# Optimization experiments

Measured on AMD Instinct MI355X. Metric: run time of the kernel, lower is better.

The kernel has to match this reference:

```python
import jax, jax.numpy as jnp
import numpy as np

B, T, C, H = 4, 2048, 1024, 16
D = C // H  # head_size = 64


def setup_inputs() -> dict:
    key = jax.random.key(0)
    k1, k2, k3 = jax.random.split(key, 3)
    x = jax.random.normal(k1, (B, T, C), dtype=jnp.float32)
    w_qkv = jax.random.normal(k2, (C, 3 * C), dtype=jnp.float32) * (C ** -0.5)
    b_qkv = jnp.zeros((3 * C,), dtype=jnp.float32)
    w_proj = jax.random.normal(k3, (C, C), dtype=jnp.float32) * (C ** -0.5)
    b_proj = jnp.zeros((C,), dtype=jnp.float32)
    return {"x": x, "w_qkv": w_qkv, "b_qkv": b_qkv, "w_proj": w_proj, "b_proj": b_proj}


def reference(x, w_qkv, b_qkv, w_proj, b_proj):
    b, t, c = x.shape
    qkv = x @ w_qkv + b_qkv                      # [B,T,3C]
    q, k, v = jnp.split(qkv, 3, axis=-1)
    # [B,T,C] -> [B,H,T,D]
    q = q.reshape(b, t, H, D).transpose(0, 2, 1, 3)
    k = k.reshape(b, t, H, D).transpose(0, 2, 1, 3)
    v = v.reshape(b, t, H, D).transpose(0, 2, 1, 3)
    attn = jnp.einsum('bhqd,bhkd->bhqk', q, k) * (D ** -0.5)
    causal = jnp.tril(jnp.ones((t, t), dtype=bool))
    attn = jnp.where(causal[None, None], attn, -jnp.inf)
    attn = jax.nn.softmax(attn, axis=-1)
    # dropout: eval mode (identity)
    out = jnp.einsum('bhqk,bhkd->bhqd', attn, v)
    out = out.transpose(0, 2, 1, 3).reshape(b, t, c)
    return out @ w_proj + b_proj
```

## Files before the change

### kernel.cpp

```cpp
#include <hip/hip_runtime.h>

#define B_ 4
#define T_ 2048
#define C_ 1024
#define H_ 16
#define D_ 64

typedef __attribute__((ext_vector_type(8))) short short8;
typedef __attribute__((ext_vector_type(4))) float f32x4;

__device__ inline unsigned short f2bf(float f) {
    union { float f; unsigned u; } v; v.f = f;
    unsigned r = v.u + 0x7fffu + ((v.u >> 16) & 1u);
    return (unsigned short)(r >> 16);
}

__device__ inline unsigned int pk_bf16(float a, float b) {
#if __has_builtin(__builtin_amdgcn_cvt_pk_bf16_f32)
    typedef __attribute__((ext_vector_type(2))) __bf16 bf16x2;
    bf16x2 v = __builtin_amdgcn_cvt_pk_bf16_f32(a, b);
    return __builtin_bit_cast(unsigned int, v);
#else
    return (unsigned)f2bf(a) | ((unsigned)f2bf(b) << 16);
#endif
}

__device__ inline void async_ld16(const void* g, void* lds) {
    __builtin_amdgcn_global_load_lds(
        (const __attribute__((address_space(1))) unsigned int*)g,
        (__attribute__((address_space(3))) unsigned int*)lds, 16, 0, 0);
}

#define MFMA_BF16 __builtin_amdgcn_mfma_f32_16x16x32_bf16

__global__ __launch_bounds__(256) void prep_all(
    const float* __restrict__ x, const float* __restrict__ w_qkv,
    const float* __restrict__ w_proj,
    unsigned short* __restrict__ xb, unsigned short* __restrict__ wqkvT,
    unsigned short* __restrict__ wprojT)
{
    const int bid = blockIdx.x;
    if (bid < 8192) {
        int i = (bid * 256 + threadIdx.x) * 4;
        float4 v = *(const float4*)(x + i);
        uint2 o;
        o.x = pk_bf16(v.x, v.y);
        o.y = pk_bf16(v.z, v.w);
        *(uint2*)(xb + i) = o;
        return;
    }
    __shared__ float tile[32][33];
    const int tt = bid - 8192;
    int bx = tt & 127;
    const int by = tt >> 7;
    const float* src; unsigned short* dst; int Cc;
    if (bx < 96) { src = w_qkv;  dst = wqkvT;  Cc = 3072; }
    else         { src = w_proj; dst = wprojT; Cc = 1024; bx -= 96; }
    const int tx = threadIdx.x & 31, ty = threadIdx.x >> 5;
    #pragma unroll
    for (int r = 0; r < 32; r += 8)
        tile[ty + r][tx] = src[(size_t)(by*32 + ty + r) * Cc + bx*32 + tx];
    __syncthreads();
    #pragma unroll
    for (int r = 0; r < 32; r += 8)
        dst[(size_t)(bx*32 + ty + r) * 1024 + by*32 + tx] = f2bf(tile[tx][ty + r]);
}

__global__ __launch_bounds__(256) void gemm_qkv(
    const unsigned short* __restrict__ A,
    const unsigned short* __restrict__ BT,
    const float* __restrict__ bias,
    unsigned short* __restrict__ qb, unsigned short* __restrict__ kb,
    unsigned short* __restrict__ vtb)
{
    __shared__ unsigned short As[128 * 64];
    __shared__ unsigned short Bs[128 * 64];
    const int tid = threadIdx.x;
    const int wave = tid >> 6, lane = tid & 63;
    const int wm = wave >> 1, wn = wave & 1;
    const int l15 = lane & 15, lq = lane >> 4;
    const int bid = blockIdx.x;
    const int xcd = bid & 7, idx = bid >> 3;
    const int m0 = (xcd * 8 + (idx & 7)) * 128;
    const int n0 = (idx >> 3) * 128;
    const int sel = n0 >> 10;
    const int row8 = lane >> 3;
    const int chx8 = ((lane & 7) ^ row8) * 8;
    const int cxa = l15 & 7;

    f32x4 acc[4][4] = {};

    for (int k0 = 0; k0 < 1024; k0 += 64) {
        #pragma unroll
        for (int c = 0; c < 4; ++c) {
            const int r = wave*32 + c*8;
            async_ld16(A  + (size_t)(m0 + r + row8)*1024 + k0 + chx8,
                       (char*)As + r*128);
            async_ld16(BT + (size_t)(n0 + r + row8)*1024 + k0 + chx8,
                       (char*)Bs + r*128);
        }
        __syncthreads();
        #pragma unroll
        for (int ks = 0; ks < 2; ++ks) {
            short8 af[4], bf[4];
            #pragma unroll
            for (int i = 0; i < 4; ++i) {
                const int ra = wm*64 + i*16 + l15;
                const int rb = wn*64 + i*16 + l15;
                af[i] = *(const short8*)&As[ra*64 + (((ks*4 + lq) ^ cxa) << 3)];
                bf[i] = *(const short8*)&Bs[rb*64 + (((ks*4 + lq) ^ cxa) << 3)];
            }
            if (sel < 2) {
                #pragma unroll
                for (int mi = 0; mi < 4; ++mi)
                    #pragma unroll
                    for (int ni = 0; ni < 4; ++ni)
                        acc[mi][ni] = MFMA_BF16(bf[ni], af[mi], acc[mi][ni], 0, 0, 0);
            } else {
                #pragma unroll
                for (int mi = 0; mi < 4; ++mi)
                    #pragma unroll
                    for (int ni = 0; ni < 4; ++ni)
                        acc[mi][ni] = MFMA_BF16(af[mi], bf[ni], acc[mi][ni], 0, 0, 0);
            }
        }
        __syncthreads();
    }

    if (sel < 2) {
        const float qs = (sel == 0) ? 0.180336880f : 1.0f;
        unsigned short* dst = (sel == 0) ? qb : kb;
        #pragma unroll
        for (int mi = 0; mi < 4; ++mi) {
            const int t = m0 + wm*64 + mi*16 + l15;
            const int bb = t >> 11, tt = t & 2047;
            #pragma unroll
            for (int ni = 0; ni < 4; ++ni) {
                const int nb = n0 + wn*64 + ni*16 + lq*4;
                const int hh = (nb >> 6) & 15, d0 = nb & 63;
                float4 bv = *(const float4*)(bias + nb);
                float v0 = (acc[mi][ni][0] + bv.x) * qs;
                float v1 = (acc[mi][ni][1] + bv.y) * qs;
                float v2 = (acc[mi][ni][2] + bv.z) * qs;
                float v3 = (acc[mi][ni][3] + bv.w) * qs;
                uint2 pk; pk.x = pk_bf16(v0, v1); pk.y = pk_bf16(v2, v3);
                *(uint2*)(dst + ((size_t)(bb*16 + hh)*2048 + tt)*64 + d0) = pk;
            }
        }
    } else {
        #pragma unroll
        for (int mi = 0; mi < 4; ++mi) {
            const int t0 = m0 + wm*64 + mi*16 + lq*4;
            const int bb = t0 >> 11, tt = t0 & 2047;
            const int tl = tt & 63;
            const int tp = (tt & ~63) | (tl & 32) | ((tl & 12) << 1) | ((tl & 16) >> 2);
            #pragma unroll
            for (int ni = 0; ni < 4; ++ni) {
                const int n = n0 + wn*64 + ni*16 + l15;
                const int hh = (n >> 6) & 15, d = n & 63;
                const float bs = bias[n];
                uint2 pk;
                pk.x = pk_bf16(acc[mi][ni][0] + bs, acc[mi][ni][1] + bs);
                pk.y = pk_bf16(acc[mi][ni][2] + bs, acc[mi][ni][3] + bs);
                *(uint2*)(vtb + ((size_t)(bb*16 + hh)*64 + d)*2048 + tp) = pk;
            }
        }
    }
}

__global__ __launch_bounds__(256) void gemm_proj(
    const unsigned short* __restrict__ A,
    const unsigned short* __restrict__ BT,
    const float* __restrict__ bias,
    float* __restrict__ out)
{
    __shared__ unsigned short As[128 * 64];
    __shared__ unsigned short Bs[128 * 64];
    const int tid = threadIdx.x;
    const int wave = tid >> 6, lane = tid & 63;
    const int wm = wave >> 1, wn = wave & 1;
    const int l15 = lane & 15, lq = lane >> 4;
    const int bid = blockIdx.x;
    const int xcd = bid & 7, idx = bid >> 3;
    const int m0 = (xcd * 8 + (idx & 7)) * 128;
    const int n0 = (idx >> 3) * 128;
    const int row8 = lane >> 3;
    const int chx8 = ((lane & 7) ^ row8) * 8;
    const int cxa = l15 & 7;

    f32x4 acc[4][4] = {};

    for (int k0 = 0; k0 < 1024; k0 += 64) {
        #pragma unroll
        for (int c = 0; c < 4; ++c) {
            const int r = wave*32 + c*8;
            async_ld16(A  + (size_t)(m0 + r + row8)*1024 + k0 + chx8,
                       (char*)As + r*128);
            async_ld16(BT + (size_t)(n0 + r + row8)*1024 + k0 + chx8,
                       (char*)Bs + r*128);
        }
        __syncthreads();
        #pragma unroll
        for (int ks = 0; ks < 2; ++ks) {
            short8 af[4], bf[4];
            #pragma unroll
            for (int i = 0; i < 4; ++i) {
                const int ra = wm*64 + i*16 + l15;
                const int rb = wn*64 + i*16 + l15;
                af[i] = *(const short8*)&As[ra*64 + (((ks*4 + lq) ^ cxa) << 3)];
                bf[i] = *(const short8*)&Bs[rb*64 + (((ks*4 + lq) ^ cxa) << 3)];
            }
            #pragma unroll
            for (int mi = 0; mi < 4; ++mi)
                #pragma unroll
                for (int ni = 0; ni < 4; ++ni)
                    acc[mi][ni] = MFMA_BF16(bf[ni], af[mi], acc[mi][ni], 0, 0, 0);
        }
        __syncthreads();
    }

    #pragma unroll
    for (int mi = 0; mi < 4; ++mi) {
        const int m = m0 + wm*64 + mi*16 + l15;
        #pragma unroll
        for (int ni = 0; ni < 4; ++ni) {
            const int nb = n0 + wn*64 + ni*16 + lq*4;
            float4 bv = *(const float4*)(bias + nb);
            float4 o;
            o.x = acc[mi][ni][0] + bv.x;
            o.y = acc[mi][ni][1] + bv.y;
            o.z = acc[mi][ni][2] + bv.z;
            o.w = acc[mi][ni][3] + bv.w;
            *(float4*)(out + (size_t)m * 1024 + nb) = o;
        }
    }
}

__global__ __launch_bounds__(256, 2) void attn_mfma(
    const unsigned short* __restrict__ qb,
    const unsigned short* __restrict__ kb,
    const unsigned short* __restrict__ vtb,
    unsigned short* __restrict__ ab)
{
    extern __shared__ unsigned char smem[];
    const int tid  = threadIdx.x;
    const int wave = tid >> 6, lane = tid & 63;
    const int l15  = lane & 15, lq = lane >> 4;
    const int linear = blockIdx.x;
    const int xc  = linear & 7;
    const int idx = linear >> 3;
    const int bh  = xc * 8 + (idx & 7);
    const int qblk = 31 - (idx >> 3);
    const int q0 = qblk * 64;
    const int b = bh >> 4, h = bh & 15;
    const size_t base = (size_t)bh * 2048 * 64;

    unsigned short* Kw = (unsigned short*)(smem + wave * 16384);
    unsigned short* Vw = Kw + 4096;

    const int row8 = lane >> 3;
    const int chx8 = ((lane & 7) ^ row8) * 8;

#define STAGE_K(J0) do { _Pragma("unroll") for (int op = 0; op < 8; ++op) \
    async_ld16(kb + base + (size_t)((J0) + op*8 + row8)*64 + chx8, \
               (char*)Kw + op*1024); } while (0)
#define STAGE_V(J0) do { _Pragma("unroll") for (int op = 0; op < 8; ++op) \
    async_ld16(vtb + base + (size_t)(op*8 + row8)*2048 + (J0) + chx8, \
               (char*)Vw + op*1024); } while (0)

    short8 qf[2][4];
    #pragma unroll
    for (int ks = 0; ks < 2; ++ks)
        #pragma unroll
        for (int nq = 0; nq < 4; ++nq)
            qf[ks][nq] = *(const short8*)(qb + base
                + (size_t)(q0 + nq*16 + l15)*64 + ks*32 + lq*8);

    f32x4 o[4][4] = {};
    float lacc[4] = {0.f, 0.f, 0.f, 0.f};

    const int jfirst = wave * 64;
    const int nt = (qblk >= wave) ? ((qblk - wave) >> 2) + 1 : 0;

    if (nt > 0) { STAGE_K(jfirst); STAGE_V(jfirst); }

    for (int i = 0; i < nt; ++i) {
        const int j0 = jfirst + i * 256;
        const bool more = (i + 1 < nt);

        asm volatile("s_waitcnt vmcnt(8)" ::: "memory");

        short8 kf0[4], kf1[4];
        #pragma unroll
        for (int ni = 0; ni < 4; ++ni) {
            const unsigned short* kr = Kw + (ni*16 + l15) * 64;
            kf0[ni] = *(const short8*)(kr + (((0*4 + lq) ^ (l15 & 7)) << 3));
            kf1[ni] = *(const short8*)(kr + (((1*4 + lq) ^ (l15 & 7)) << 3));
        }
        f32x4 s[4][4] = {};
        #pragma unroll
        for (int ni = 0; ni < 4; ++ni)
            #pragma unroll
            for (int nq = 0; nq < 4; ++nq) {
                s[ni][nq] = MFMA_BF16(kf0[ni], qf[0][nq], s[ni][nq], 0, 0, 0);
                s[ni][nq] = MFMA_BF16(kf1[ni], qf[1][nq], s[ni][nq], 0, 0, 0);
            }
        asm volatile("s_waitcnt lgkmcnt(0)" ::: "memory");
        if (more) STAGE_K(j0 + 256);

        if (j0 == q0) {
            #pragma unroll
            for (int ni = 0; ni < 4; ++ni)
                #pragma unroll
                for (int nq = 0; nq < 4; ++nq)
                    #pragma unroll
                    for (int r = 0; r < 4; ++r)
                        if (ni*16 + lq*4 + r > nq*16 + l15)
                            s[ni][nq][r] = -1e30f;
        }

        short8 pf[2][4];
        #pragma unroll
        for (int c = 0; c < 2; ++c)
            #pragma unroll
            for (int nq = 0; nq < 4; ++nq) {
                float p0 = __builtin_amdgcn_exp2f(s[2*c  ][nq][0]);
                float p1 = __builtin_amdgcn_exp2f(s[2*c  ][nq][1]);
                float p2 = __builtin_amdgcn_exp2f(s[2*c  ][nq][2]);
                float p3 = __builtin_amdgcn_exp2f(s[2*c  ][nq][3]);
                float p4 = __builtin_amdgcn_exp2f(s[2*c+1][nq][0]);
                float p5 = __builtin_amdgcn_exp2f(s[2*c+1][nq][1]);
                float p6 = __builtin_amdgcn_exp2f(s[2*c+1][nq][2]);
                float p7 = __builtin_amdgcn_exp2f(s[2*c+1][nq][3]);
                lacc[nq] += ((p0 + p1) + (p2 + p3)) + ((p4 + p5) + (p6 + p7));
                uint4 pu;
                pu.x = pk_bf16(p0, p1); pu.y = pk_bf16(p2, p3);
                pu.z = pk_bf16(p4, p5); pu.w = pk_bf16(p6, p7);
                pf[c][nq] = __builtin_bit_cast(short8, pu);
            }

        if (more) asm volatile("s_waitcnt vmcnt(8)" ::: "memory");
        else      asm volatile("s_waitcnt vmcnt(0)" ::: "memory");

        #pragma unroll
        for (int c = 0; c < 2; ++c) {
            short8 vf[4];
            #pragma unroll
            for (int nd = 0; nd < 4; ++nd)
                vf[nd] = *(const short8*)(Vw + (nd*16 + l15) * 64
                    + (((c*4 + lq) ^ (l15 & 7)) << 3));
            #pragma unroll
            for (int nq = 0; nq < 4; ++nq)
                #pragma unroll
                for (int nd = 0; nd < 4; ++nd)
                    o[nq][nd] = MFMA_BF16(pf[c][nq], vf[nd], o[nq][nd], 0, 0, 0);
        }
        asm volatile("s_waitcnt lgkmcnt(0)" ::: "memory");
        if (more) STAGE_V(j0 + 256);
    }
#undef STAGE_K
#undef STAGE_V

    #pragma unroll
    for (int nq = 0; nq < 4; ++nq) {
        float t = lacc[nq];
        t += __shfl_xor(t, 16);
        t += __shfl_xor(t, 32);
        if (lq == 0) ((float*)Kw)[nq*16 + l15] = t;
    }
    __syncthreads();
    const int qg = wave, d = lane;
    f32x4 linv4[4];
    #pragma unroll
    for (int j = 0; j < 4; ++j) {
        f32x4 lsum = {};
        #pragma unroll
        for (int w2 = 0; w2 < 4; ++w2)
            lsum += *(const f32x4*)((const float*)(smem + w2*16384) + qg*16 + j*4);
        #pragma unroll
        for (int r = 0; r < 4; ++r)
            linv4[j][r] = __builtin_amdgcn_rcpf(lsum[r]);
    }
    __syncthreads();
    #pragma unroll
    for (int nq = 0; nq < 4; ++nq)
        #pragma unroll
        for (int nd = 0; nd < 4; ++nd) {
            const int row = nd*16 + l15;
            const int col = (nq*16 + lq*4 + 4*l15) & 63;
            *(f32x4*)((float*)Kw + row*64 + col) = o[nq][nd];
        }
    __syncthreads();
    #pragma unroll
    for (int j = 0; j < 4; ++j) {
        const int colb = (qg*16 + j*4 + 4*(d & 15)) & 63;
        f32x4 acc = {};
        #pragma unroll
        for (int w2 = 0; w2 < 4; ++w2)
            acc += *(const f32x4*)((const float*)(smem + w2*16384) + d*64 + colb);
        #pragma unroll
        for (int r = 0; r < 4; ++r) {
            const int q = qg*16 + j*4 + r;
            ab[(size_t)(b*2048 + q0 + q)*1024 + h*64 + d] = f2bf(acc[r] * linv4[j][r]);
        }
    }
}

extern "C" void kernel_launch(void* const* d_in, const int* in_sizes, int n_in,
                              void* d_out, int out_size, void* d_ws, size_t ws_size,
                              hipStream_t stream) {
    const float* x      = (const float*)d_in[0];
    const float* w_qkv  = (const float*)d_in[1];
    const float* b_qkv  = (const float*)d_in[2];
    const float* w_proj = (const float*)d_in[3];
    const float* b_proj = (const float*)d_in[4];
    float* out = (float*)d_out;

    unsigned short* xb     = (unsigned short*)d_ws;
    unsigned short* wqkvT  = xb + 8388608;
    unsigned short* wprojT = wqkvT + 3145728;
    unsigned short* qbuf   = wprojT + 1048576;
    unsigned short* kbuf   = qbuf + 8388608;
    unsigned short* vtbuf  = kbuf + 8388608;
    unsigned short* abuf   = vtbuf + 8388608;

    prep_all<<<12288, 256, 0, stream>>>(x, w_qkv, w_proj, xb, wqkvT, wprojT);
    gemm_qkv<<<1536, 256, 0, stream>>>(xb, wqkvT, b_qkv, qbuf, kbuf, vtbuf);
    attn_mfma<<<2048, 256, 65536, stream>>>(qbuf, kbuf, vtbuf, abuf);
    gemm_proj<<<512, 256, 0, stream>>>(abuf, wprojT, b_proj, out);
}
```

Measured before the change: 239.0 us.

## Double-buffer LDS tiles in QKV and projection GEMMs to overlap loads

Both GEMM kernels now use two shared-memory buffers for the A and B tiles. The next K-tile is prefetched with async loads while MFMAs run on the current tile, and one barrier per iteration is removed. The aim is to hide global-memory latency behind compute. In exchange, LDS use per block doubles to 64KB, which may limit occupancy.

Result: no change. 237.7 us (median of 2 runs) (-0.5%).

```diff
diff --git a/kernel.cpp b/kernel.cpp
--- a/kernel.cpp
+++ b/kernel.cpp
@@ -73,8 +73,8 @@
     unsigned short* __restrict__ qb, unsigned short* __restrict__ kb,
     unsigned short* __restrict__ vtb)
 {
-    __shared__ unsigned short As[128 * 64];
-    __shared__ unsigned short Bs[128 * 64];
+    __shared__ unsigned short As[2][128 * 64];
+    __shared__ unsigned short Bs[2][128 * 64];
     const int tid = threadIdx.x;
     const int wave = tid >> 6, lane = tid & 63;
     const int wm = wave >> 1, wn = wave & 1;
@@ -90,16 +90,23 @@
 
     f32x4 acc[4][4] = {};
 
-    for (int k0 = 0; k0 < 1024; k0 += 64) {
-        #pragma unroll
-        for (int c = 0; c < 4; ++c) {
-            const int r = wave*32 + c*8;
-            async_ld16(A  + (size_t)(m0 + r + row8)*1024 + k0 + chx8,
-                       (char*)As + r*128);
-            async_ld16(BT + (size_t)(n0 + r + row8)*1024 + k0 + chx8,
-                       (char*)Bs + r*128);
-        }
-        __syncthreads();
+#define STAGE(buf, K0) do { _Pragma("unroll") \
+    for (int c = 0; c < 4; ++c) { \
+        const int r = wave*32 + c*8; \
+        async_ld16(A  + (size_t)(m0 + r + row8)*1024 + (K0) + chx8, \
+                   (char*)&As[buf][0] + r*128); \
+        async_ld16(BT + (size_t)(n0 + r + row8)*1024 + (K0) + chx8, \
+                   (char*)&Bs[buf][0] + r*128); \
+    } } while (0)
+
+    STAGE(0, 0);
+    __syncthreads();
+
+    for (int t = 0; t < 16; ++t) {
+        const int cur = t & 1;
+        if (t < 15) STAGE(cur ^ 1, (t + 1) << 6);
+        const unsigned short* Ac = &As[cur][0];
+        const unsigned short* Bc = &Bs[cur][0];
         #pragma unroll
         for (int ks = 0; ks < 2; ++ks) {
             short8 af[4], bf[4];
@@ -107,8 +114,8 @@
             for (int i = 0; i < 4; ++i) {
                 const int ra = wm*64 + i*16 + l15;
                 const int rb = wn*64 + i*16 + l15;
-                af[i] = *(const short8*)&As[ra*64 + (((ks*4 + lq) ^ cxa) << 3)];
-                bf[i] = *(const short8*)&Bs[rb*64 + (((ks*4 + lq) ^ cxa) << 3)];
+                af[i] = *(const short8*)&Ac[ra*64 + (((ks*4 + lq) ^ cxa) << 3)];
+                bf[i] = *(const short8*)&Bc[rb*64 + (((ks*4 + lq) ^ cxa) << 3)];
             }
             if (sel < 2) {
                 #pragma unroll
@@ -126,6 +133,7 @@
         }
         __syncthreads();
     }
+#undef STAGE
 
     if (sel < 2) {
         const float qs = (sel == 0) ? 0.180336880f : 1.0f;
@@ -174,8 +182,8 @@
     const float* __restrict__ bias,
     float* __restrict__ out)
 {
-    __shared__ unsigned short As[128 * 64];
-    __shared__ unsigned short Bs[128 * 64];
+    __shared__ unsigned short As[2][128 * 64];
+    __shared__ unsigned short Bs[2][128 * 64];
     const int tid = threadIdx.x;
     const int wave = tid >> 6, lane = tid & 63;
     const int wm = wave >> 1, wn = wave & 1;
@@ -190,16 +198,23 @@
 
     f32x4 acc[4][4] = {};
 
-    for (int k0 = 0; k0 < 1024; k0 += 64) {
-        #pragma unroll
-        for (int c = 0; c < 4; ++c) {
-            const int r = wave*32 + c*8;
-            async_ld16(A  + (size_t)(m0 + r + row8)*1024 + k0 + chx8,
-                       (char*)As + r*128);
-            async_ld16(BT + (size_t)(n0 + r + row8)*1024 + k0 + chx8,
-                       (char*)Bs + r*128);
-        }
-        __syncthreads();
+#define PSTAGE(buf, K0) do { _Pragma("unroll") \
+    for (int c = 0; c < 4; ++c) { \
+        const int r = wave*32 + c*8; \
+        async_ld16(A  + (size_t)(m0 + r + row8)*1024 + (K0) + chx8, \
+                   (char*)&As[buf][0] + r*128); \
+        async_ld16(BT + (size_t)(n0 + r + row8)*1024 + (K0) + chx8, \
+                   (char*)&Bs[buf][0] + r*128); \
+    } } while (0)
+
+    PSTAGE(0, 0);
+    __syncthreads();
+
+    for (int t = 0; t < 16; ++t) {
+        const int cur = t & 1;
+        if (t < 15) PSTAGE(cur ^ 1, (t + 1) << 6);
+        const unsigned short* Ac = &As[cur][0];
+        const unsigned short* Bc = &Bs[cur][0];
         #pragma unroll
         for (int ks = 0; ks < 2; ++ks) {
             short8 af[4], bf[4];
@@ -207,8 +222,8 @@
             for (int i = 0; i < 4; ++i) {
                 const int ra = wm*64 + i*16 + l15;
                 const int rb = wn*64 + i*16 + l15;
-                af[i] = *(const short8*)&As[ra*64 + (((ks*4 + lq) ^ cxa) << 3)];
-                bf[i] = *(const short8*)&Bs[rb*64 + (((ks*4 + lq) ^ cxa) << 3)];
+                af[i] = *(const short8*)&Ac[ra*64 + (((ks*4 + lq) ^ cxa) << 3)];
+                bf[i] = *(const short8*)&Bc[rb*64 + (((ks*4 + lq) ^ cxa) << 3)];
             }
             #pragma unroll
             for (int mi = 0; mi < 4; ++mi)
@@ -218,6 +233,7 @@
         }
         __syncthreads();
     }
+#undef PSTAGE
 
     #pragma unroll
     for (int mi = 0; mi < 4; ++mi) {
```
